# Optimization experiments

Hardware: AMD Instinct MI355X
Metric: run time of the kernel (lower is better)

## Reference

```python
import jax, jax.numpy as jnp
import numpy as np

IN_C, OUT_C, K, STRIDE, PAD = 64, 128, 3, 1, 1


def setup_inputs() -> dict:
    key = jax.random.key(0)
    kx, kw = jax.random.split(key)
    x = jax.random.normal(kx, (16, IN_C, 112, 112), dtype=jnp.float32)
    scale = np.sqrt(2.0 / (IN_C * K * K)).astype(np.float32)
    weight = jax.random.normal(kw, (OUT_C, IN_C, K, K), dtype=jnp.float32) * scale
    bias = jnp.zeros((OUT_C,), dtype=jnp.float32)
    return {"x": x, "weight": weight, "bias": bias}


def reference(x, weight, bias):
    # Direct 2D convolution (cross-correlation, like torch Conv2d), NCHW layout.
    out = jax.lax.conv_general_dilated(
        x, weight,
        window_strides=(STRIDE, STRIDE),
        padding=((PAD, PAD), (PAD, PAD)),
        dimension_numbers=("NCHW", "OIHW", "NCHW"),
    )
    return out + bias[None, :, None, None]
```

## Files before the change

kernel.cpp:

```cpp
#include <hip/hip_runtime.h>
#include <stdint.h>


#define HW     112
#define PIX    12544
#define ICN    64
#define OCN    128
#define TILEP  128
#define PTILES 98
#define NBLK   1568
#define NIMG   16

#define XT_BYTES   (NIMG * PIX * ICN * 2)
#define WT_OFF     XT_BYTES
#define WT_BYTES   (9 * OCN * ICN * 2)
#define ZG_OFF     (WT_OFF + WT_BYTES)
#define XBLK       (NIMG * (PIX / 64))
#define WBLK       72

typedef __attribute__((ext_vector_type(8))) __bf16 bf16x8;
typedef __attribute__((ext_vector_type(4))) float  f32x4;

__device__ __forceinline__ uint32_t rne_lo(float f) {
    uint32_t u = __builtin_bit_cast(uint32_t, f);
    return (u + 0x7fffu + ((u >> 16) & 1u)) >> 16;
}
__device__ __forceinline__ uint32_t pk2(float a, float b) {
    uint32_t ub = __builtin_bit_cast(uint32_t, b);
    ub = (ub + 0x7fffu + ((ub >> 16) & 1u)) & 0xffff0000u;
    return rne_lo(a) | ub;
}

__device__ __forceinline__ void load_lds16(const void* g, void* l) {
    __builtin_amdgcn_global_load_lds(
        (const __attribute__((address_space(1))) uint32_t*)g,
        (__attribute__((address_space(3))) uint32_t*)l, 16, 0, 0);
}

__global__ void __launch_bounds__(256)
prep(const float* __restrict__ x, const float* __restrict__ w, uint8_t* __restrict__ ws) {
    const int b = blockIdx.x;
    const int t = threadIdx.x;
    uint16_t* xt = (uint16_t*)ws;
    uint16_t* wt = (uint16_t*)(ws + WT_OFF);

    if (b < XBLK) {
        const int n  = b / (PIX / 64);
        const int p0 = (b - n * (PIX / 64)) * 64;
        const int px = t >> 2;
        const int q  = t & 3;
        const float* src = x + ((size_t)n * ICN + q * 16) * PIX + p0 + px;
        float v[16];
#pragma unroll
        for (int i = 0; i < 16; ++i) v[i] = src[(size_t)i * PIX];
        uint4 u0 = make_uint4(pk2(v[0], v[1]),  pk2(v[2], v[3]),
                              pk2(v[4], v[5]),  pk2(v[6], v[7]));
        uint4 u1 = make_uint4(pk2(v[8], v[9]),  pk2(v[10], v[11]),
                              pk2(v[12], v[13]), pk2(v[14], v[15]));
        char* dst = (char*)xt + ((size_t)(n * PIX + p0 + px)) * 128 + q * 32;
        *(uint4*)dst        = u0;
        *(uint4*)(dst + 16) = u1;
    } else {
        const int wb = b - XBLK;
#pragma unroll
        for (int k = 0; k < 4; ++k) {
            int wi = wb * 1024 + k * 256 + t;
            int r  = wi >> 13;
            int oc = (wi >> 6) & 127;
            int ic = wi & 63;
            wt[wi] = (uint16_t)rne_lo(w[oc * 576 + ic * 9 + r]);
        }
        if (wb == 0 && t < 8) ((uint4*)(ws + ZG_OFF))[t] = make_uint4(0, 0, 0, 0);
    }
}

__global__ void __launch_bounds__(256)
conv_mfma(const uint8_t* __restrict__ ws, const float* __restrict__ bias,
          float* __restrict__ out) {
    __shared__ uint16_t As[8192];
    __shared__ uint16_t Xs[8192];

    const char* xt = (const char*)ws;
    const char* wt = (const char*)(ws + WT_OFF);
    const char* zg = (const char*)(ws + ZG_OFF);

    const int t = threadIdx.x;
    const int b = blockIdx.x;
    const int n_img = b / PTILES;
    const int p0 = (b - n_img * PTILES) * TILEP;

    const int lane = t & 63;
    const int wave = t >> 6;
    const int lr = lane & 15;
    const int lq = lane >> 4;
    const int oc_base = (wave & 1) * 64;
    const int px_base = (wave >> 1) * 64;

    const int rowB = t >> 3;
    const int cswz = (t & 7) ^ (rowB & 7);
    int sh[4], sw[4];
    const char* xaddr[4];
#pragma unroll
    for (int r2 = 0; r2 < 4; ++r2) {
        int row = r2 * 32 + rowB;
        int p = p0 + row;
        int hh = p / HW;
        sh[r2] = hh;
        sw[r2] = p - hh * HW;
        xaddr[r2] = xt + ((size_t)(n_img * PIX + p)) * 128 + cswz * 16;
    }
    const char* waddr0 = wt + rowB * 128 + cswz * 16;
    const char* zaddr  = zg + (t & 7) * 16;

    f32x4 acc[4][4];
    {
        f32x4 z = {0.f, 0.f, 0.f, 0.f};
#pragma unroll
        for (int i = 0; i < 4; ++i)
#pragma unroll
            for (int j = 0; j < 4; ++j) acc[i][j] = z;
    }

#pragma unroll
    for (int tap = 0; tap < 9; ++tap) {
        const int dy = tap / 3 - 1;
        const int dx = tap - (tap / 3) * 3 - 1;
        const int toff = (dy * HW + dx) * 128;

        __syncthreads();

#pragma unroll
        for (int r2 = 0; r2 < 4; ++r2)
            load_lds16(waddr0 + tap * 16384 + r2 * 4096,
                       (char*)As + r2 * 4096 + wave * 1024);
#pragma unroll
        for (int r2 = 0; r2 < 4; ++r2) {
            int hh = sh[r2] + dy;
            int wwp = sw[r2] + dx;
            bool ok = ((unsigned)hh < HW) & ((unsigned)wwp < HW);
            const char* gp = ok ? (xaddr[r2] + toff) : zaddr;
            load_lds16(gp, (char*)Xs + r2 * 4096 + wave * 1024);
        }

        __syncthreads();

#pragma unroll
        for (int kh = 0; kh < 2; ++kh) {
            bf16x8 a_frag[4], b_frag[4];
            const int cc = kh * 4 + lq;
#pragma unroll
            for (int mi = 0; mi < 4; ++mi) {
                int R = oc_base + mi * 16 + lr;
                a_frag[mi] = *(const bf16x8*)((const char*)As + R * 128 + ((cc ^ (R & 7)) * 16));
            }
#pragma unroll
            for (int ni = 0; ni < 4; ++ni) {
                int R = px_base + ni * 16 + lr;
                b_frag[ni] = *(const bf16x8*)((const char*)Xs + R * 128 + ((cc ^ (R & 7)) * 16));
            }
#pragma unroll
            for (int mi = 0; mi < 4; ++mi)
#pragma unroll
                for (int ni = 0; ni < 4; ++ni)
                    acc[mi][ni] = __builtin_amdgcn_mfma_f32_16x16x32_bf16(
                        a_frag[mi], b_frag[ni], acc[mi][ni], 0, 0, 0);
        }
    }

#pragma unroll
    for (int mi = 0; mi < 4; ++mi) {
#pragma unroll
        for (int rg = 0; rg < 4; ++rg) {
            const int oc = oc_base + mi * 16 + lq * 4 + rg;
            const float bb = bias[oc];
            float* orow = out + ((size_t)n_img * OCN + oc) * PIX + p0 + px_base + lr;
#pragma unroll
            for (int ni = 0; ni < 4; ++ni)
                orow[ni * 16] = acc[mi][ni][rg] + bb;
        }
    }
}

extern "C" void kernel_launch(void* const* d_in, const int* in_sizes, int n_in,
                              void* d_out, int out_size, void* d_ws, size_t ws_size,
                              hipStream_t stream) {
    const float* x    = (const float*)d_in[0];
    const float* w    = (const float*)d_in[1];
    const float* bias = (const float*)d_in[2];
    float* out = (float*)d_out;
    uint8_t* ws = (uint8_t*)d_ws;

    prep<<<XBLK + WBLK, 256, 0, stream>>>(x, w, ws);
    conv_mfma<<<NBLK, 256, 0, stream>>>(ws, bias, out);
}
```

Measured before the change: 173.8 us.

## Stage input halo in LDS once and double-buffer per-tap weights

Each block now loads its 128-pixel tile plus a one-row halo above and below (about 354 rows of 64 bf16 channels) into LDS once. The nine taps read shifted rows from that buffer instead of re-fetching nine shifted tiles from global memory, and out-of-bounds positions point to a dedicated zero row. Weights for the next tap are prefetched into a second LDS buffer while the current tap computes, which drops from two barriers per tap to one. The cost is a larger LDS footprint, roughly 77KB per block, which lowers the number of blocks that can be resident per CU. The halo load is also not overlapped with compute.

```diff
diff --git a/kernel.cpp b/kernel.cpp
--- a/kernel.cpp
+++ b/kernel.cpp
@@ -17,6 +17,11 @@
 #define ZG_OFF     (WT_OFF + WT_BYTES)
 #define XBLK       (NIMG * (PIX / 64))
 #define WBLK       72
+
+#define XU_LO      113
+#define XU_DATA    354
+#define XU_ZROW    354
+#define XU_ROWS    355
 
 typedef __attribute__((ext_vector_type(8))) __bf16 bf16x8;
 typedef __attribute__((ext_vector_type(4))) float  f32x4;
@@ -77,8 +82,8 @@
 __global__ void __launch_bounds__(256)
 conv_mfma(const uint8_t* __restrict__ ws, const float* __restrict__ bias,
           float* __restrict__ out) {
-    __shared__ uint16_t As[8192];
-    __shared__ uint16_t Xs[8192];
+    __shared__ uint8_t Wb[2][16384];
+    __shared__ uint8_t Xu[XU_ROWS * 128];
 
     const char* xt = (const char*)ws;
     const char* wt = (const char*)(ws + WT_OFF);
@@ -96,21 +101,40 @@
     const int oc_base = (wave & 1) * 64;
     const int px_base = (wave >> 1) * 64;
 
-    const int rowB = t >> 3;
-    const int cswz = (t & 7) ^ (rowB & 7);
-    int sh[4], sw[4];
-    const char* xaddr[4];
-#pragma unroll
-    for (int r2 = 0; r2 < 4; ++r2) {
-        int row = r2 * 32 + rowB;
-        int p = p0 + row;
-        int hh = p / HW;
-        sh[r2] = hh;
-        sw[r2] = p - hh * HW;
-        xaddr[r2] = xt + ((size_t)(n_img * PIX + p)) * 128 + cswz * 16;
-    }
-    const char* waddr0 = wt + rowB * 128 + cswz * 16;
-    const char* zaddr  = zg + (t & 7) * 16;
+    const int rowB  = t >> 3;
+    const int cswz8 = ((t & 7) ^ (rowB & 7)) * 16;
+    const char* zaddr = zg + (t & 7) * 16;
+
+    const char* xrow0 = xt + ((ptrdiff_t)(n_img * PIX + p0 - XU_LO)) * 128 + cswz8;
+#pragma unroll
+    for (int r2 = 0; r2 < 11; ++r2) {
+        int r = r2 * 32 + rowB;
+        int p = p0 - XU_LO + r;
+        const char* gp = ((unsigned)p < PIX) ? (xrow0 + (ptrdiff_t)r * 128) : zaddr;
+        load_lds16(gp, (char*)Xu + r2 * 4096 + wave * 1024);
+    }
+    if (t < 16) {
+        int r = 352 + (t >> 3);
+        int p = p0 - XU_LO + r;
+        const char* gp = ((unsigned)p < PIX) ? (xrow0 + (ptrdiff_t)r * 128) : zaddr;
+        load_lds16(gp, (char*)Xu + 352 * 128);
+    }
+    if (t < 8) *(uint4*)((char*)Xu + XU_ZROW * 128 + t * 16) = make_uint4(0, 0, 0, 0);
+
+    const char* wsrc = wt + rowB * 128 + cswz8;
+#pragma unroll
+    for (int r2 = 0; r2 < 4; ++r2)
+        load_lds16(wsrc + r2 * 4096, (char*)Wb + r2 * 4096 + wave * 1024);
+
+    int hh[4], wwp[4], rb[4];
+#pragma unroll
+    for (int ni = 0; ni < 4; ++ni) {
+        int p = p0 + px_base + ni * 16 + lr;
+        int h = p / HW;
+        hh[ni]  = h;
+        wwp[ni] = p - h * HW;
+        rb[ni]  = px_base + ni * 16 + lr + XU_LO;
+    }
 
     f32x4 acc[4][4];
     {
@@ -121,43 +145,42 @@
             for (int j = 0; j < 4; ++j) acc[i][j] = z;
     }
 
+    __syncthreads();
+
 #pragma unroll
     for (int tap = 0; tap < 9; ++tap) {
         const int dy = tap / 3 - 1;
         const int dx = tap - (tap / 3) * 3 - 1;
-        const int toff = (dy * HW + dx) * 128;
-
-        __syncthreads();
-
-#pragma unroll
-        for (int r2 = 0; r2 < 4; ++r2)
-            load_lds16(waddr0 + tap * 16384 + r2 * 4096,
-                       (char*)As + r2 * 4096 + wave * 1024);
-#pragma unroll
-        for (int r2 = 0; r2 < 4; ++r2) {
-            int hh = sh[r2] + dy;
-            int wwp = sw[r2] + dx;
-            bool ok = ((unsigned)hh < HW) & ((unsigned)wwp < HW);
-            const char* gp = ok ? (xaddr[r2] + toff) : zaddr;
-            load_lds16(gp, (char*)Xs + r2 * 4096 + wave * 1024);
-        }
-
-        __syncthreads();
-
+        const int roff = dy * HW + dx;
+
+        if (tap < 8) {
+#pragma unroll
+            for (int r2 = 0; r2 < 4; ++r2)
+                load_lds16(wsrc + (tap + 1) * 16384 + r2 * 4096,
+                           (char*)Wb + ((tap + 1) & 1) * 16384 + r2 * 4096 + wave * 1024);
+        }
+
+        int ro[4];
+#pragma unroll
+        for (int ni = 0; ni < 4; ++ni) {
+            bool ok = ((unsigned)(hh[ni] + dy) < HW) & ((unsigned)(wwp[ni] + dx) < HW);
+            ro[ni] = ok ? (rb[ni] + roff) : XU_ZROW;
+        }
+
+        const char* wbase = (const char*)Wb + (tap & 1) * 16384;
 #pragma unroll
         for (int kh = 0; kh < 2; ++kh) {
+            const int cc = kh * 4 + lq;
             bf16x8 a_frag[4], b_frag[4];
-            const int cc = kh * 4 + lq;
 #pragma unroll
             for (int mi = 0; mi < 4; ++mi) {
                 int R = oc_base + mi * 16 + lr;
-                a_frag[mi] = *(const bf16x8*)((const char*)As + R * 128 + ((cc ^ (R & 7)) * 16));
+                a_frag[mi] = *(const bf16x8*)(wbase + R * 128 + ((cc ^ (R & 7)) * 16));
             }
 #pragma unroll
-            for (int ni = 0; ni < 4; ++ni) {
-                int R = px_base + ni * 16 + lr;
-                b_frag[ni] = *(const bf16x8*)((const char*)Xs + R * 128 + ((cc ^ (R & 7)) * 16));
-            }
+            for (int ni = 0; ni < 4; ++ni)
+                b_frag[ni] = *(const bf16x8*)((const char*)Xu + ro[ni] * 128
+                                              + ((cc ^ (ro[ni] & 7)) * 16));
 #pragma unroll
             for (int mi = 0; mi < 4; ++mi)
 #pragma unroll
@@ -165,6 +188,7 @@
                     acc[mi][ni] = __builtin_amdgcn_mfma_f32_16x16x32_bf16(
                         a_frag[mi], b_frag[ni], acc[mi][ni], 0, 0, 0);
         }
+        if (tap < 8) __syncthreads();
     }
 
 #pragma unroll
```

Measured after the change: 179.6 us. 3.3% more time.
